# Performance work log

Hardware: AMD Instinct MI355X
Metric: run time of the kernel (lower is better)

Reference implementation:

```python
import jax, jax.numpy as jnp
import numpy as np

N = 100000
D = 256
E = 1600000
H, C = 2, 32  # heads, out_channels


def setup_inputs() -> dict:
    key = jax.random.key(0)
    ks = jax.random.split(key, 10)
    h_x = jax.random.normal(ks[0], (N, D), dtype=jnp.float32)
    t_x = jax.random.normal(ks[1], (N, D), dtype=jnp.float32)
    src = jax.random.randint(ks[2], (E,), 0, N, dtype=jnp.int32)
    off = jax.random.randint(ks[3], (E,), 1, N, dtype=jnp.int32)
    dst = (src + off) % N  # guarantees src != dst (remove_self_loops is a no-op)
    edge_index = jnp.stack([src, dst])  # [2, E]
    enrichment_weights = jax.random.uniform(ks[4], (E,), dtype=jnp.float32) * 3.0
    s = 1.0 / np.sqrt(D)
    W_src = jax.random.normal(ks[5], (D, H * C), dtype=jnp.float32) * s
    W_dst = jax.random.normal(ks[6], (D, H * C), dtype=jnp.float32) * s
    att_src = jax.random.normal(ks[7], (H, C), dtype=jnp.float32) * 0.1
    att_dst = jax.random.normal(ks[8], (H, C), dtype=jnp.float32) * 0.1
    bias = jnp.zeros((H * C,), dtype=jnp.float32)
    enrichment_scale = jnp.float32(0.5)
    return {"h_x": h_x, "t_x": t_x, "edge_index": edge_index,
            "enrichment_weights": enrichment_weights,
            "W_src": W_src, "W_dst": W_dst, "att_src": att_src,
            "att_dst": att_dst, "bias": bias,
            "enrichment_scale": enrichment_scale}


def _gat(x_src, x_dst, src, dst, num_dst, W_src, W_dst, att_src, att_dst, bias):
    # PyG GATConv, bipartite, heads=H, out=C, concat=True, eval mode
    hs = (x_src @ W_src).reshape(-1, H, C)  # [Ns, H, C]
    hd = (x_dst @ W_dst).reshape(-1, H, C)  # [Nd, H, C]
    a_s = jnp.einsum('nhc,hc->nh', hs, att_src)  # [Ns, H]
    a_d = jnp.einsum('nhc,hc->nh', hd, att_dst)  # [Nd, H]
    alpha = jax.nn.leaky_relu(a_s[src] + a_d[dst], 0.2)  # [E', H]
    m = jax.ops.segment_max(alpha, dst, num_segments=num_dst)
    alpha = jnp.exp(alpha - m[dst])
    z = jax.ops.segment_sum(alpha, dst, num_segments=num_dst)
    alpha = alpha / (z[dst] + 1e-16)
    msg = hs[src] * alpha[:, :, None]  # [E', H, C]
    out = jax.ops.segment_sum(msg, dst, num_segments=num_dst)  # [Nd, H, C]
    return out.reshape(num_dst, H * C) + bias


def reference(h_x, t_x, edge_index, enrichment_weights,
              W_src, W_dst, att_src, att_dst, bias, enrichment_scale):
    h_in = jax.nn.elu(h_x)
    t_in = jax.nn.elu(t_x)
    src, dst = edge_index[0], edge_index[1]
    loops = jnp.arange(min(h_x.shape[0], t_x.shape[0]), dtype=src.dtype)
    # direction 1: (h -> t), PyG appends self-loops after the input edges
    s1 = jnp.concatenate([src, loops]); d1 = jnp.concatenate([dst, loops])
    t_rep = _gat(h_in, t_in, s1, d1, t_x.shape[0], W_src, W_dst, att_src, att_dst, bias)
    # direction 2: reversed edges (t -> h)
    s2 = jnp.concatenate([dst, loops]); d2 = jnp.concatenate([src, loops])
    h_rep = _gat(t_in, h_in, s2, d2, h_x.shape[0], W_src, W_dst, att_src, att_dst, bias)
    # edge-enrichment reweighting (scalar factor)
    scale = 0.5 * jnp.tanh(enrichment_scale)
    ew = jnp.clip(enrichment_weights, 0.3, 3.0)
    aw = jax.nn.softmax(ew)
    weighted = jnp.sum(aw * ew)
    factor = 1.0 + scale * (weighted - 1.0)
    return (h_rep * factor, t_rep * factor)
```

## Files before the change

### kernel.cpp

```cpp
#include <hip/hip_runtime.h>
#include <math.h>

typedef __attribute__((ext_vector_type(8))) short bf16x8;
typedef __attribute__((ext_vector_type(4))) float f32x4;

__device__ __forceinline__ float bf2f(unsigned short u) {
    union { unsigned int i; float f; } c;
    c.i = ((unsigned int)u) << 16;
    return c.f;
}
__device__ __forceinline__ unsigned short f2bf(float f) {
    union { float f; unsigned int i; } c;
    c.f = f;
    unsigned int b = c.i + 0x7FFFu + ((c.i >> 16) & 1u);
    return (unsigned short)(b >> 16);
}
__device__ __forceinline__ float eluf(float v) {
    return v > 0.f ? v : (__expf(v) - 1.f);
}
__device__ __forceinline__ float lrelu(float v) {
    return v >= 0.f ? v : 0.2f * v;
}

__global__ void detect_kernel(const unsigned int* __restrict__ w, int nwords,
                              int* __restrict__ flag)
{
    __shared__ int cnt_s;
    if (threadIdx.x == 0) cnt_s = 0;
    __syncthreads();
    int sane = 0;
    for (int i = threadIdx.x; i < nwords; i += 256) {
        unsigned int lo = w[i] & 0xffffu;
        int e = (int)((lo >> 7) & 0xffu);
        if (e >= 114 && e <= 136) sane++;
    }
    atomicAdd(&cnt_s, sane);
    __syncthreads();
    if (threadIdx.x == 0) *flag = (2 * cnt_s > nwords) ? 1 : 0;
}

__global__ __launch_bounds__(256) void wfrag_kernel(
    const unsigned short* __restrict__ Wsrc, const unsigned short* __restrict__ Wdst,
    const int* __restrict__ flag, unsigned short* __restrict__ Wfrag)
{
    if (!*flag) return;
    const int nch = 8 * 8 * 64;
    for (int ch = blockIdx.x * 256 + threadIdx.x; ch < nch; ch += gridDim.x * 256) {
        int l  = ch & 63;
        int t  = (ch >> 6) & 7;
        int ks = ch >> 9;
        int col = t * 16 + (l & 15);
        int k0  = ks * 32 + (l >> 4) * 8;
        const unsigned short* W = (col < 64) ? (Wsrc + col) : (Wdst + (col - 64));
#pragma unroll
        for (int j = 0; j < 8; ++j)
            Wfrag[(size_t)ch * 8 + j] = W[(size_t)(k0 + j) * 64];
    }
}

__global__ __launch_bounds__(256) void gemm_mfma_kernel(
    const void* __restrict__ xh, const void* __restrict__ xt,
    const unsigned short* __restrict__ Wfrag,
    const void* __restrict__ att_src, const void* __restrict__ att_dst,
    const int* __restrict__ flag,
    float* __restrict__ P, float* __restrict__ as_all, float* __restrict__ ad_all,
    int N)
{
    if (!*flag) return;
    const unsigned short* xv = (const unsigned short*)((blockIdx.y == 0) ? xh : xt);
    float* Pout = P + (size_t)blockIdx.y * (size_t)N * 64u;
    float* asO  = as_all + (size_t)blockIdx.y * (size_t)N * 2u;
    float* adO  = ad_all + (size_t)blockIdx.y * (size_t)N * 2u;
    const int tid = threadIdx.x;
    const int w   = tid >> 6;
    const int l   = tid & 63;
    const int l15 = l & 15;
    const int lhi = l >> 4;
    const int rowA = blockIdx.x * 64 + w * 16 + l15;
    const bool rv = rowA < N;

    bf16x8 a[8];
#pragma unroll
    for (int ks = 0; ks < 8; ++ks) {
        union { bf16x8 v; unsigned int u[4]; } o;
        if (rv) {
            uint4 raw = *(const uint4*)(xv + (size_t)rowA * 256 + ks * 32 + lhi * 8);
            unsigned int wsr[4] = {raw.x, raw.y, raw.z, raw.w};
#pragma unroll
            for (int i = 0; i < 4; ++i) {
                float lo = eluf(bf2f((unsigned short)(wsr[i] & 0xffffu)));
                float hi = eluf(bf2f((unsigned short)(wsr[i] >> 16)));
                o.u[i] = (unsigned int)f2bf(lo) | ((unsigned int)f2bf(hi) << 16);
            }
        } else {
            o.u[0] = o.u[1] = o.u[2] = o.u[3] = 0u;
        }
        a[ks] = o.v;
    }

    f32x4 acc[8];
#pragma unroll
    for (int t = 0; t < 8; ++t) acc[t] = (f32x4){0.f, 0.f, 0.f, 0.f};

    const bf16x8* wf = (const bf16x8*)Wfrag;
#pragma unroll
    for (int ks = 0; ks < 8; ++ks) {
#pragma unroll
        for (int t = 0; t < 8; ++t) {
            bf16x8 b = wf[(ks * 8 + t) * 64 + l];
            acc[t] = __builtin_amdgcn_mfma_f32_16x16x32_bf16(a[ks], b, acc[t], 0, 0, 0);
        }
    }

    float asv[4], adv[4];
#pragma unroll
    for (int t = 0; t < 4; ++t) {
        asv[t] = bf2f(((const unsigned short*)att_src)[t * 16 + l15]);
        adv[t] = bf2f(((const unsigned short*)att_dst)[t * 16 + l15]);
    }
    const int rbase = blockIdx.x * 64 + w * 16 + lhi * 4;
#pragma unroll
    for (int reg = 0; reg < 4; ++reg) {
        int row = rbase + reg;
        bool ok = row < N;
        if (ok) {
            float* p = Pout + (size_t)row * 64 + l15;
#pragma unroll
            for (int t = 0; t < 4; ++t) p[t * 16] = acc[t][reg];
        }
        float s0 = acc[0][reg] * asv[0] + acc[1][reg] * asv[1];
        float s1 = acc[2][reg] * asv[2] + acc[3][reg] * asv[3];
        float d0 = acc[4][reg] * adv[0] + acc[5][reg] * adv[1];
        float d1 = acc[6][reg] * adv[2] + acc[7][reg] * adv[3];
#pragma unroll
        for (int o2 = 8; o2 >= 1; o2 >>= 1) {
            s0 += __shfl_xor(s0, o2, 64);
            s1 += __shfl_xor(s1, o2, 64);
            d0 += __shfl_xor(d0, o2, 64);
            d1 += __shfl_xor(d1, o2, 64);
        }
        if (ok && l15 == 0) {
            asO[(size_t)row * 2 + 0] = s0;
            asO[(size_t)row * 2 + 1] = s1;
            adO[(size_t)row * 2 + 0] = d0;
            adO[(size_t)row * 2 + 1] = d1;
        }
    }
}

__global__ __launch_bounds__(256) void gemm_elu_kernel(
    const void* __restrict__ xh, const void* __restrict__ xt,
    const void* __restrict__ Wsrc, const void* __restrict__ Wdst,
    const void* __restrict__ att_src, const void* __restrict__ att_dst,
    const int* __restrict__ flag,
    float* __restrict__ P, float* __restrict__ as_all, float* __restrict__ ad_all,
    int N, int D, int skip_bf)
{
    const int isbf = *flag;
    if (skip_bf && isbf) return;
    __shared__ float xs[64][33];
    __shared__ float wt[32][128];
    const void* xv = (blockIdx.y == 0) ? xh : xt;
    float* Pout = P + (size_t)blockIdx.y * (size_t)N * 64u;
    float* asO  = as_all + (size_t)blockIdx.y * (size_t)N * 2u;
    float* adO  = ad_all + (size_t)blockIdx.y * (size_t)N * 2u;
    const int rowBase = blockIdx.x * 64;
    const int tid = threadIdx.x;
    const int tcx = tid & 15;
    const int tcy = tid >> 4;

    float acc[4][8];
#pragma unroll
    for (int r = 0; r < 4; ++r)
#pragma unroll
        for (int c = 0; c < 8; ++c) acc[r][c] = 0.f;

    for (int kc = 0; kc < D; kc += 32) {
        {
            int row = tid >> 2;
            int kq  = (tid & 3) * 8;
            int r = rowBase + row;
            float v[8];
            if (r < N) {
                if (isbf) {
                    const unsigned short* xb = (const unsigned short*)xv;
                    uint4 raw = *(const uint4*)(xb + (size_t)r * D + kc + kq);
                    unsigned int ws[4] = {raw.x, raw.y, raw.z, raw.w};
#pragma unroll
                    for (int i = 0; i < 4; ++i) {
                        v[2 * i]     = bf2f((unsigned short)(ws[i] & 0xffffu));
                        v[2 * i + 1] = bf2f((unsigned short)(ws[i] >> 16));
                    }
                } else {
                    const float* xf = (const float*)xv;
                    const float4* p4 = (const float4*)(xf + (size_t)r * D + kc + kq);
                    float4 f0 = p4[0], f1 = p4[1];
                    v[0] = f0.x; v[1] = f0.y; v[2] = f0.z; v[3] = f0.w;
                    v[4] = f1.x; v[5] = f1.y; v[6] = f1.z; v[7] = f1.w;
                }
#pragma unroll
                for (int i = 0; i < 8; ++i) v[i] = eluf(v[i]);
            } else {
#pragma unroll
                for (int i = 0; i < 8; ++i) v[i] = 0.f;
            }
#pragma unroll
            for (int i = 0; i < 8; ++i) xs[row][kq + i] = v[i];
        }
#pragma unroll
        for (int i = 0; i < 2; ++i) {
            int f = (tid + i * 256) * 8;
            int k = f >> 7;
            int c = f & 127;
            float v[8];
            if (isbf) {
                const unsigned short* Wp = (c < 64)
                    ? ((const unsigned short*)Wsrc + (size_t)(kc + k) * 64 + c)
                    : ((const unsigned short*)Wdst + (size_t)(kc + k) * 64 + (c - 64));
                uint4 raw = *(const uint4*)Wp;
                unsigned int ws[4] = {raw.x, raw.y, raw.z, raw.w};
#pragma unroll
                for (int q = 0; q < 4; ++q) {
                    v[2 * q]     = bf2f((unsigned short)(ws[q] & 0xffffu));
                    v[2 * q + 1] = bf2f((unsigned short)(ws[q] >> 16));
                }
            } else {
                const float* Wp = (c < 64)
                    ? ((const float*)Wsrc + (size_t)(kc + k) * 64 + c)
                    : ((const float*)Wdst + (size_t)(kc + k) * 64 + (c - 64));
                const float4* p4 = (const float4*)Wp;
                float4 f0 = p4[0], f1 = p4[1];
                v[0] = f0.x; v[1] = f0.y; v[2] = f0.z; v[3] = f0.w;
                v[4] = f1.x; v[5] = f1.y; v[6] = f1.z; v[7] = f1.w;
            }
#pragma unroll
            for (int q = 0; q < 8; ++q) wt[k][c + q] = v[q];
        }
        __syncthreads();
#pragma unroll 8
        for (int k = 0; k < 32; ++k) {
            float xr[4];
#pragma unroll
            for (int r = 0; r < 4; ++r) xr[r] = xs[tcy * 4 + r][k];
            float4 w0 = *(const float4*)&wt[k][tcx * 8];
            float4 w1 = *(const float4*)&wt[k][tcx * 8 + 4];
#pragma unroll
            for (int r = 0; r < 4; ++r) {
                acc[r][0] += xr[r] * w0.x; acc[r][1] += xr[r] * w0.y;
                acc[r][2] += xr[r] * w0.z; acc[r][3] += xr[r] * w0.w;
                acc[r][4] += xr[r] * w1.x; acc[r][5] += xr[r] * w1.y;
                acc[r][6] += xr[r] * w1.z; acc[r][7] += xr[r] * w1.w;
            }
        }
        __syncthreads();
    }

    float attv[8];
#pragma unroll
    for (int q = 0; q < 8; ++q) {
        int c = tcx * 8 + q;
        if (isbf) attv[q] = (c < 64) ? bf2f(((const unsigned short*)att_src)[c])
                                     : bf2f(((const unsigned short*)att_dst)[c - 64]);
        else      attv[q] = (c < 64) ? ((const float*)att_src)[c]
                                     : ((const float*)att_dst)[c - 64];
    }

#pragma unroll
    for (int r = 0; r < 4; ++r) {
        int row = rowBase + tcy * 4 + r;
        bool ok = row < N;
        if (ok && tcx < 8) {
            float* p = Pout + (size_t)row * 64 + tcx * 8;
            *(float4*)p       = make_float4(acc[r][0], acc[r][1], acc[r][2], acc[r][3]);
            *(float4*)(p + 4) = make_float4(acc[r][4], acc[r][5], acc[r][6], acc[r][7]);
        }
        float part = 0.f;
#pragma unroll
        for (int q = 0; q < 8; ++q) part += acc[r][q] * attv[q];
        part += __shfl_xor(part, 1, 64);
        part += __shfl_xor(part, 2, 64);
        if (ok && (tcx & 3) == 0) {
            if (tcx == 0)       asO[(size_t)row * 2 + 0] = part;
            else if (tcx == 4)  asO[(size_t)row * 2 + 1] = part;
            else if (tcx == 8)  adO[(size_t)row * 2 + 0] = part;
            else                adO[(size_t)row * 2 + 1] = part;
        }
    }
}

__global__ void count_kernel(const int* __restrict__ srce, const int* __restrict__ dste,
                             int* __restrict__ cnt, int N, int E)
{
    int e = blockIdx.x * blockDim.x + threadIdx.x;
    if (e >= E) return;
    atomicAdd(&cnt[dste[e]], 1);
    atomicAdd(&cnt[N + srce[e]], 1);
}

__global__ __launch_bounds__(256) void scan_bsum_kernel(
    const int* __restrict__ cnt, int M, int chunk, int* __restrict__ bsum)
{
    __shared__ int r[4];
    int beg = blockIdx.x * chunk;
    int end = beg + chunk; if (end > M) end = M;
    int s = 0;
    for (int i = beg + threadIdx.x; i < end; i += 256) s += cnt[i];
#pragma unroll
    for (int o = 32; o >= 1; o >>= 1) s += __shfl_down(s, o, 64);
    int lane = threadIdx.x & 63, wv = threadIdx.x >> 6;
    if (lane == 0) r[wv] = s;
    __syncthreads();
    if (threadIdx.x == 0) bsum[blockIdx.x] = r[0] + r[1] + r[2] + r[3];
}

__global__ __launch_bounds__(256) void scan_boff_kernel(
    const int* __restrict__ bsum, int NB, int* __restrict__ boff)
{
    __shared__ int s[256];
    int t = threadIdx.x;
    int v = (t < NB) ? bsum[t] : 0;
    s[t] = v;
    __syncthreads();
    for (int o = 1; o < 256; o <<= 1) {
        int x = (t >= o) ? s[t - o] : 0;
        __syncthreads();
        s[t] += x;
        __syncthreads();
    }
    if (t < NB) boff[t] = s[t] - v;
}

__global__ __launch_bounds__(256) void scan_write_kernel(
    const int* __restrict__ cnt, int M, int chunk,
    const int* __restrict__ boff, int* __restrict__ off)
{
    __shared__ int s[256];
    int t = threadIdx.x;
    int beg = blockIdx.x * chunk;
    int end = beg + chunk; if (end > M) end = M;
    if (beg >= M) return;
    int running = boff[blockIdx.x];
    for (int base = beg; base < end; base += 256) {
        int i = base + t;
        int v = (i < end) ? cnt[i] : 0;
        s[t] = v;
        __syncthreads();
        for (int o = 1; o < 256; o <<= 1) {
            int x = (t >= o) ? s[t - o] : 0;
            __syncthreads();
            s[t] += x;
            __syncthreads();
        }
        if (i < end) off[i] = running + s[t] - v;
        int total = s[255];
        __syncthreads();
        running += total;
    }
    if (end == M && t == 0) off[M] = running;
}

__global__ void fill_kernel(const int* __restrict__ srce, const int* __restrict__ dste,
                            const int* __restrict__ off, int* __restrict__ cur,
                            int* __restrict__ idx, int N, int E)
{
    int e = blockIdx.x * blockDim.x + threadIdx.x;
    if (e >= E) return;
    int s = srce[e], d = dste[e];
    int p  = atomicAdd(&cur[d], 1);
    idx[off[d] + p] = s;
    int p2 = atomicAdd(&cur[N + s], 1);
    idx[off[N + s] + p2] = d;
}

__global__ __launch_bounds__(256) void enrich_kernel(
    const void* __restrict__ ew, const int* __restrict__ flag,
    float* __restrict__ S, int E)
{
    __shared__ float r1[4], r2[4];
    const int isbf = *flag;
    float e1 = 0.f, e2 = 0.f;
    for (int i = blockIdx.x * 256 + threadIdx.x; i < E; i += gridDim.x * 256) {
        float c = isbf ? bf2f(((const unsigned short*)ew)[i]) : ((const float*)ew)[i];
        c = fminf(fmaxf(c, 0.3f), 3.0f);
        float ex = __expf(c);
        e1 += ex;
        e2 += c * ex;
    }
#pragma unroll
    for (int o = 32; o >= 1; o >>= 1) {
        e1 += __shfl_down(e1, o, 64);
        e2 += __shfl_down(e2, o, 64);
    }
    int lane = threadIdx.x & 63;
    int wv = threadIdx.x >> 6;
    if (lane == 0) { r1[wv] = e1; r2[wv] = e2; }
    __syncthreads();
    if (threadIdx.x == 0) {
        atomicAdd(&S[0], r1[0] + r1[1] + r1[2] + r1[3]);
        atomicAdd(&S[1], r2[0] + r2[1] + r2[2] + r2[3]);
    }
}

__global__ __launch_bounds__(256) void agg_kernel(
    const int* __restrict__ off, const int* __restrict__ idx,
    const float* __restrict__ as_all, const float* __restrict__ ad_all,
    const float* __restrict__ Pall,
    const void* __restrict__ bias,
    const float* __restrict__ S,
    const void* __restrict__ esc,
    const int* __restrict__ flag,
    void* __restrict__ out, int N)
{
    const int isbf = *flag;
    int q = (blockIdx.x * 256 + threadIdx.x) >> 6;
    int lane = threadIdx.x & 63;
    if (q >= 2 * N) return;
    int dir = (q >= N) ? 1 : 0;
    int n = q - dir * N;
    const float* a_s  = as_all + (size_t)dir * 2u * (size_t)N;
    const float* a_d  = ad_all + (size_t)(1 - dir) * 2u * (size_t)N;
    const float* Psrc = Pall + (size_t)dir * (size_t)N * 64u;
    size_t outOff = dir ? 0u : (size_t)N * 64u;
    const int jb = off[q], je = off[q + 1];

    float2 adv2 = *(const float2*)(a_d + (size_t)n * 2);
    float2 ass2 = *(const float2*)(a_s + (size_t)n * 2);
    float self0 = lrelu(ass2.x + adv2.x);
    float self1 = lrelu(ass2.y + adv2.y);

    float m0 = self0, m1 = self1;
    for (int j = jb + lane; j < je; j += 64) {
        int sidx = idx[j];
        float2 as2 = *(const float2*)(a_s + (size_t)sidx * 2);
        m0 = fmaxf(m0, lrelu(as2.x + adv2.x));
        m1 = fmaxf(m1, lrelu(as2.y + adv2.y));
    }
#pragma unroll
    for (int o = 32; o >= 1; o >>= 1) {
        m0 = fmaxf(m0, __shfl_xor(m0, o, 64));
        m1 = fmaxf(m1, __shfl_xor(m1, o, 64));
    }

    const int hi = lane >> 5;
    const float m    = hi ? m1 : m0;
    const float adv  = hi ? adv2.y : adv2.x;
    const float pSelf = __expf((hi ? self1 : self0) - m);
    float z   = pSelf;
    float acc = pSelf * Psrc[(size_t)n * 64 + lane];
    for (int j = jb; j < je; ++j) {
        int sidx = idx[j];
        float2 as2 = *(const float2*)(a_s + (size_t)sidx * 2);
        float alf = lrelu((hi ? as2.y : as2.x) + adv);
        float p = __expf(alf - m);
        z += p;
        acc = fmaf(p, Psrc[(size_t)sidx * 64 + lane], acc);
    }

    float escv = isbf ? bf2f(((const unsigned short*)esc)[0]) : ((const float*)esc)[0];
    float bv   = isbf ? bf2f(((const unsigned short*)bias)[lane]) : ((const float*)bias)[lane];
    float weighted = S[1] / S[0];
    float factor = 1.f + 0.5f * tanhf(escv) * (weighted - 1.f);
    float o = (acc / (z + 1e-16f) + bv) * factor;
    size_t oi = outOff + (size_t)n * 64 + lane;
    if (isbf) ((unsigned short*)out)[oi] = f2bf(o);
    else      ((float*)out)[oi] = o;
}

extern "C" void kernel_launch(void* const* d_in, const int* in_sizes, int n_in,
                              void* d_out, int out_size, void* d_ws, size_t ws_size,
                              hipStream_t stream)
{
    const void* hx      = d_in[0];
    const void* tx      = d_in[1];
    const int*  eidx    = (const int*)d_in[2];
    const void* ew      = d_in[3];
    const void* Wsrc    = d_in[4];
    const void* Wdst    = d_in[5];
    const void* att_src = d_in[6];
    const void* att_dst = d_in[7];
    const void* bias    = d_in[8];
    const void* esc     = d_in[9];

    const int HC = in_sizes[6];
    const int D  = in_sizes[4] / HC;
    const int N  = in_sizes[0] / D;
    const int E  = in_sizes[3];
    const int* srce = eidx;
    const int* dste = eidx + E;

    const bool canM = (D == 256) && (HC == 64);
    const int skipBf = canM ? 1 : 0;

    char* wsb = (char*)d_ws;
    size_t o = 0;
    auto alloc = [&](size_t bytes) -> void* {
        void* p = wsb + o;
        o += (bytes + 255) & ~(size_t)255;
        return p;
    };
    float* Pall   = (float*)alloc((size_t)2 * N * 64 * 4);
    float* as_all = (float*)alloc((size_t)2 * N * 2 * 4);
    float* ad_all = (float*)alloc((size_t)2 * N * 2 * 4);
    float* S      = (float*)alloc(2 * 4);
    int*   cnt    = (int*)alloc((size_t)2 * N * 4);
    int*   offp   = (int*)alloc(((size_t)2 * N + 1) * 4);
    int*   cur    = (int*)alloc((size_t)2 * N * 4);
    int*   idx    = (int*)alloc((size_t)2 * E * 4);
    int*   flag   = (int*)alloc(256);
    int*   bsum   = (int*)alloc(256 * 4);
    int*   boff   = (int*)alloc(256 * 4);
    unsigned short* Wfrag = (unsigned short*)alloc((size_t)8 * 8 * 64 * 8 * 2);

    hipMemsetAsync(cnt, 0, (size_t)2 * N * 4, stream);
    hipMemsetAsync(cur, 0, (size_t)2 * N * 4, stream);
    hipMemsetAsync(S, 0, 2 * 4, stream);

    detect_kernel<<<1, 256, 0, stream>>>((const unsigned int*)hx, 65536, flag);

    dim3 gGemm((N + 63) / 64, 2);
    if (canM) {
        wfrag_kernel<<<16, 256, 0, stream>>>((const unsigned short*)Wsrc,
                                             (const unsigned short*)Wdst, flag, Wfrag);
        gemm_mfma_kernel<<<gGemm, 256, 0, stream>>>(hx, tx, Wfrag, att_src, att_dst,
                                                    flag, Pall, as_all, ad_all, N);
    }
    gemm_elu_kernel<<<gGemm, 256, 0, stream>>>(hx, tx, Wsrc, Wdst, att_src, att_dst,
                                               flag, Pall, as_all, ad_all, N, D, skipBf);
    count_kernel<<<(E + 255) / 256, 256, 0, stream>>>(srce, dste, cnt, N, E);

    const int M = 2 * N;
    int chunk = (M + 255) / 256;
    chunk = (chunk + 255) & ~255;
    const int NB = (M + chunk - 1) / chunk;
    scan_bsum_kernel<<<NB, 256, 0, stream>>>(cnt, M, chunk, bsum);
    scan_boff_kernel<<<1, 256, 0, stream>>>(bsum, NB, boff);
    scan_write_kernel<<<NB, 256, 0, stream>>>(cnt, M, chunk, boff, offp);

    fill_kernel<<<(E + 255) / 256, 256, 0, stream>>>(srce, dste, offp, cur, idx, N, E);
    enrich_kernel<<<512, 256, 0, stream>>>(ew, flag, S, E);

    agg_kernel<<<(2 * N + 3) / 4, 256, 0, stream>>>(offp, idx, as_all, ad_all,
                                                    Pall, bias, S, esc, flag,
                                                    d_out, N);
}
```

Baseline: 1.088 ms.

## Store projections in fp16, use global max shift, unroll aggregation loop

```diff
diff --git a/kernel.cpp b/kernel.cpp
--- a/kernel.cpp
+++ b/kernel.cpp
@@ -1,4 +1,5 @@
 #include <hip/hip_runtime.h>
+#include <hip/hip_fp16.h>
 #include <math.h>
 
 typedef __attribute__((ext_vector_type(8))) short bf16x8;
@@ -20,6 +21,15 @@
 }
 __device__ __forceinline__ float lrelu(float v) {
     return v >= 0.f ? v : 0.2f * v;
+}
+__device__ __forceinline__ unsigned int fenc(float f) {
+    union { float f; unsigned int u; } c; c.f = f;
+    return (c.u & 0x80000000u) ? ~c.u : (c.u | 0x80000000u);
+}
+__device__ __forceinline__ float fdec(unsigned int k) {
+    union { float f; unsigned int u; } c;
+    c.u = (k & 0x80000000u) ? (k ^ 0x80000000u) : ~k;
+    return c.f;
 }
 
 __global__ void detect_kernel(const unsigned int* __restrict__ w, int nwords,
@@ -63,12 +73,12 @@
     const unsigned short* __restrict__ Wfrag,
     const void* __restrict__ att_src, const void* __restrict__ att_dst,
     const int* __restrict__ flag,
-    float* __restrict__ P, float* __restrict__ as_all, float* __restrict__ ad_all,
+    __half* __restrict__ P, float* __restrict__ as_all, float* __restrict__ ad_all,
     int N)
 {
     if (!*flag) return;
     const unsigned short* xv = (const unsigned short*)((blockIdx.y == 0) ? xh : xt);
-    float* Pout = P + (size_t)blockIdx.y * (size_t)N * 64u;
+    __half* Pout = P + (size_t)blockIdx.y * (size_t)N * 64u;
     float* asO  = as_all + (size_t)blockIdx.y * (size_t)N * 2u;
     float* adO  = ad_all + (size_t)blockIdx.y * (size_t)N * 2u;
     const int tid = threadIdx.x;
@@ -124,9 +134,9 @@
         int row = rbase + reg;
         bool ok = row < N;
         if (ok) {
-            float* p = Pout + (size_t)row * 64 + l15;
-#pragma unroll
-            for (int t = 0; t < 4; ++t) p[t * 16] = acc[t][reg];
+            __half* p = Pout + (size_t)row * 64 + l15;
+#pragma unroll
+            for (int t = 0; t < 4; ++t) p[t * 16] = __float2half(acc[t][reg]);
         }
         float s0 = acc[0][reg] * asv[0] + acc[1][reg] * asv[1];
         float s1 = acc[2][reg] * asv[2] + acc[3][reg] * asv[3];
@@ -153,7 +163,7 @@
     const void* __restrict__ Wsrc, const void* __restrict__ Wdst,
     const void* __restrict__ att_src, const void* __restrict__ att_dst,
     const int* __restrict__ flag,
-    float* __restrict__ P, float* __restrict__ as_all, float* __restrict__ ad_all,
+    __half* __restrict__ P, float* __restrict__ as_all, float* __restrict__ ad_all,
     int N, int D, int skip_bf)
 {
     const int isbf = *flag;
@@ -161,7 +171,7 @@
     __shared__ float xs[64][33];
     __shared__ float wt[32][128];
     const void* xv = (blockIdx.y == 0) ? xh : xt;
-    float* Pout = P + (size_t)blockIdx.y * (size_t)N * 64u;
+    __half* Pout = P + (size_t)blockIdx.y * (size_t)N * 64u;
     float* asO  = as_all + (size_t)blockIdx.y * (size_t)N * 2u;
     float* adO  = ad_all + (size_t)blockIdx.y * (size_t)N * 2u;
     const int rowBase = blockIdx.x * 64;
@@ -270,9 +280,9 @@
         int row = rowBase + tcy * 4 + r;
         bool ok = row < N;
         if (ok && tcx < 8) {
-            float* p = Pout + (size_t)row * 64 + tcx * 8;
-            *(float4*)p       = make_float4(acc[r][0], acc[r][1], acc[r][2], acc[r][3]);
-            *(float4*)(p + 4) = make_float4(acc[r][4], acc[r][5], acc[r][6], acc[r][7]);
+            __half* p = Pout + (size_t)row * 64 + tcx * 8;
+#pragma unroll
+            for (int q = 0; q < 8; ++q) p[q] = __float2half(acc[r][q]);
         }
         float part = 0.f;
 #pragma unroll
@@ -285,6 +295,32 @@
             else if (tcx == 8)  adO[(size_t)row * 2 + 0] = part;
             else                adO[(size_t)row * 2 + 1] = part;
         }
+    }
+}
+
+__global__ __launch_bounds__(256) void gmax_kernel(
+    const float* __restrict__ as_all, unsigned int* __restrict__ gmax, int N)
+{
+    unsigned int k0 = 0, k1 = 0, k2 = 0, k3 = 0;
+    const int total = 2 * N;
+    for (int i = blockIdx.x * 256 + threadIdx.x; i < total; i += gridDim.x * 256) {
+        float2 v = *(const float2*)(as_all + (size_t)i * 2);
+        unsigned int ex = fenc(v.x), ey = fenc(v.y);
+        if (i < N) { k0 = max(k0, ex); k1 = max(k1, ey); }
+        else       { k2 = max(k2, ex); k3 = max(k3, ey); }
+    }
+#pragma unroll
+    for (int o = 32; o >= 1; o >>= 1) {
+        k0 = max(k0, (unsigned int)__shfl_xor((int)k0, o, 64));
+        k1 = max(k1, (unsigned int)__shfl_xor((int)k1, o, 64));
+        k2 = max(k2, (unsigned int)__shfl_xor((int)k2, o, 64));
+        k3 = max(k3, (unsigned int)__shfl_xor((int)k3, o, 64));
+    }
+    if ((threadIdx.x & 63) == 0) {
+        atomicMax(&gmax[0], k0);
+        atomicMax(&gmax[1], k1);
+        atomicMax(&gmax[2], k2);
+        atomicMax(&gmax[3], k3);
     }
 }
 
@@ -404,9 +440,10 @@
 __global__ __launch_bounds__(256) void agg_kernel(
     const int* __restrict__ off, const int* __restrict__ idx,
     const float* __restrict__ as_all, const float* __restrict__ ad_all,
-    const float* __restrict__ Pall,
+    const __half* __restrict__ Pall,
     const void* __restrict__ bias,
     const float* __restrict__ S,
+    const unsigned int* __restrict__ gmax,
     const void* __restrict__ esc,
     const int* __restrict__ flag,
     void* __restrict__ out, int N)
@@ -419,42 +456,43 @@
     int n = q - dir * N;
     const float* a_s  = as_all + (size_t)dir * 2u * (size_t)N;
     const float* a_d  = ad_all + (size_t)(1 - dir) * 2u * (size_t)N;
-    const float* Psrc = Pall + (size_t)dir * (size_t)N * 64u;
+    const __half* Psrc = Pall + (size_t)dir * (size_t)N * 64u;
     size_t outOff = dir ? 0u : (size_t)N * 64u;
+    const int hi = lane >> 5;
     const int jb = off[q], je = off[q + 1];
 
     float2 adv2 = *(const float2*)(a_d + (size_t)n * 2);
+    const float adv = hi ? adv2.y : adv2.x;
+    const float gm  = fdec(gmax[dir * 2 + hi]);
+    const float m   = lrelu(gm + adv);
+
     float2 ass2 = *(const float2*)(a_s + (size_t)n * 2);
-    float self0 = lrelu(ass2.x + adv2.x);
-    float self1 = lrelu(ass2.y + adv2.y);
-
-    float m0 = self0, m1 = self1;
-    for (int j = jb + lane; j < je; j += 64) {
-        int sidx = idx[j];
-        float2 as2 = *(const float2*)(a_s + (size_t)sidx * 2);
-        m0 = fmaxf(m0, lrelu(as2.x + adv2.x));
-        m1 = fmaxf(m1, lrelu(as2.y + adv2.y));
-    }
-#pragma unroll
-    for (int o = 32; o >= 1; o >>= 1) {
-        m0 = fmaxf(m0, __shfl_xor(m0, o, 64));
-        m1 = fmaxf(m1, __shfl_xor(m1, o, 64));
-    }
-
-    const int hi = lane >> 5;
-    const float m    = hi ? m1 : m0;
-    const float adv  = hi ? adv2.y : adv2.x;
-    const float pSelf = __expf((hi ? self1 : self0) - m);
-    float z   = pSelf;
-    float acc = pSelf * Psrc[(size_t)n * 64 + lane];
-    for (int j = jb; j < je; ++j) {
-        int sidx = idx[j];
-        float2 as2 = *(const float2*)(a_s + (size_t)sidx * 2);
-        float alf = lrelu((hi ? as2.y : as2.x) + adv);
-        float p = __expf(alf - m);
-        z += p;
-        acc = fmaf(p, Psrc[(size_t)sidx * 64 + lane], acc);
-    }
+    const float pSelf = __expf(lrelu((hi ? ass2.y : ass2.x) + adv) - m);
+    float z0 = pSelf, z1 = 0.f;
+    float acc0 = pSelf * __half2float(Psrc[(size_t)n * 64 + lane]);
+    float acc1 = 0.f;
+
+    int j = jb;
+    for (; j + 1 < je; j += 2) {
+        int s0 = idx[j], s1 = idx[j + 1];
+        float2 a0 = *(const float2*)(a_s + (size_t)s0 * 2);
+        float2 a1 = *(const float2*)(a_s + (size_t)s1 * 2);
+        float h0 = __half2float(Psrc[(size_t)s0 * 64 + lane]);
+        float h1 = __half2float(Psrc[(size_t)s1 * 64 + lane]);
+        float p0 = __expf(lrelu((hi ? a0.y : a0.x) + adv) - m);
+        float p1 = __expf(lrelu((hi ? a1.y : a1.x) + adv) - m);
+        z0 += p0; acc0 = fmaf(p0, h0, acc0);
+        z1 += p1; acc1 = fmaf(p1, h1, acc1);
+    }
+    if (j < je) {
+        int s0 = idx[j];
+        float2 a0 = *(const float2*)(a_s + (size_t)s0 * 2);
+        float h0 = __half2float(Psrc[(size_t)s0 * 64 + lane]);
+        float p0 = __expf(lrelu((hi ? a0.y : a0.x) + adv) - m);
+        z0 += p0; acc0 = fmaf(p0, h0, acc0);
+    }
+    float z   = z0 + z1;
+    float acc = acc0 + acc1;
 
     float escv = isbf ? bf2f(((const unsigned short*)esc)[0]) : ((const float*)esc)[0];
     float bv   = isbf ? bf2f(((const unsigned short*)bias)[lane]) : ((const float*)bias)[lane];
@@ -498,10 +536,11 @@
         o += (bytes + 255) & ~(size_t)255;
         return p;
     };
-    float* Pall   = (float*)alloc((size_t)2 * N * 64 * 4);
+    __half* Pall  = (__half*)alloc((size_t)2 * N * 64 * 2);
     float* as_all = (float*)alloc((size_t)2 * N * 2 * 4);
     float* ad_all = (float*)alloc((size_t)2 * N * 2 * 4);
     float* S      = (float*)alloc(2 * 4);
+    unsigned int* gmax = (unsigned int*)alloc(4 * 4);
     int*   cnt    = (int*)alloc((size_t)2 * N * 4);
     int*   offp   = (int*)alloc(((size_t)2 * N + 1) * 4);
     int*   cur    = (int*)alloc((size_t)2 * N * 4);
@@ -514,6 +553,7 @@
     hipMemsetAsync(cnt, 0, (size_t)2 * N * 4, stream);
     hipMemsetAsync(cur, 0, (size_t)2 * N * 4, stream);
     hipMemsetAsync(S, 0, 2 * 4, stream);
+    hipMemsetAsync(gmax, 0, 4 * 4, stream);
 
     detect_kernel<<<1, 256, 0, stream>>>((const unsigned int*)hx, 65536, flag);
 
@@ -526,6 +566,7 @@
     }
     gemm_elu_kernel<<<gGemm, 256, 0, stream>>>(hx, tx, Wsrc, Wdst, att_src, att_dst,
                                                flag, Pall, as_all, ad_all, N, D, skipBf);
+    gmax_kernel<<<256, 256, 0, stream>>>(as_all, gmax, N);
     count_kernel<<<(E + 255) / 256, 256, 0, stream>>>(srce, dste, cnt, N, E);
 
     const int M = 2 * N;
@@ -540,6 +581,6 @@
     enrich_kernel<<<512, 256, 0, stream>>>(ew, flag, S, E);
 
     agg_kernel<<<(2 * N + 3) / 4, 256, 0, stream>>>(offp, idx, as_all, ad_all,
-                                                    Pall, bias, S, esc, flag,
+                                                    Pall, bias, S, gmax, esc, flag,
                                                     d_out, N);
 }
```

Result: faster. 1.008 ms (-7.3%).
